# Performance work log

Hardware: AMD Instinct MI355X
Metric: run time of the kernel (lower is better)

## Reference

```python
import jax, jax.numpy as jnp
import numpy as np
import math

V = 32000      # vocab_size
D = 1024       # hidden_dims
T_MAX = 1024   # max_txt_len
L = 4          # n_layers
H = 8          # heads (fixed in CausalMHA)
HD = D // H
B, T = 2, 1024
EPS = 1e-5


def setup_inputs() -> dict:
    key = jax.random.key(0)
    ks = jax.random.split(key, 20)
    s = 0.02
    inp = {
        "x": jax.random.randint(ks[0], (B, T), 0, V, dtype=jnp.int64) if jax.config.read("jax_enable_x64") else jax.random.randint(ks[0], (B, T), 0, V, dtype=jnp.int32),
        "tok_emb": jax.random.normal(ks[1], (V, D), jnp.float32) * s,
        "pos_emb": jax.random.normal(ks[2], (1, T_MAX, D), jnp.float32) * s,
        "ln1_g": jnp.ones((L, D), jnp.float32),
        "ln1_b": jnp.zeros((L, D), jnp.float32),
        "wqkv": jax.random.normal(ks[3], (L, D, 3 * D), jnp.float32) * s,
        "bqkv": jnp.zeros((L, 3 * D), jnp.float32),
        "wo": jax.random.normal(ks[4], (L, D, D), jnp.float32) * s,
        "bo": jnp.zeros((L, D), jnp.float32),
        "ln2_g": jnp.ones((L, D), jnp.float32),
        "ln2_b": jnp.zeros((L, D), jnp.float32),
        "wfc": jax.random.normal(ks[5], (L, D, 4 * D), jnp.float32) * s,   # no bias
        "wfc2": jax.random.normal(ks[6], (L, 4 * D, D), jnp.float32) * s,  # no bias
        "fn_g": jnp.ones((D,), jnp.float32),
        "fn_b": jnp.zeros((D,), jnp.float32),
        "wout": jax.random.normal(ks[7], (D, V), jnp.float32) * s,
        "bout": jnp.zeros((V,), jnp.float32),
    }
    return inp


def _ln(x, g, b):
    mu = jnp.mean(x, axis=-1, keepdims=True)
    var = jnp.var(x, axis=-1, keepdims=True)
    return (x - mu) * jax.lax.rsqrt(var + EPS) * g + b


def _attn(xn, wqkv_l, bqkv_l, wo_l, bo_l):
    Bb, Tt, _ = xn.shape
    qkv = xn @ wqkv_l + bqkv_l                      # [B,T,3D]
    q, k, v = jnp.split(qkv, 3, axis=-1)
    q = q.reshape(Bb, Tt, H, HD)
    k = k.reshape(Bb, Tt, H, HD)
    v = v.reshape(Bb, Tt, H, HD)
    scores = jnp.einsum("bqhd,bkhd->bhqk", q, k) / math.sqrt(HD)
    mask = jnp.triu(jnp.ones((Tt, Tt), bool), k=1)   # True above diagonal
    scores = jnp.where(mask, jnp.float32(-jnp.inf), scores)
    att = jax.nn.softmax(scores, axis=-1)
    out = jnp.einsum("bhqk,bkhd->bqhd", att, v).reshape(Bb, Tt, D)
    return out @ wo_l + bo_l


def reference(x, tok_emb, pos_emb, ln1_g, ln1_b, wqkv, bqkv, wo, bo,
              ln2_g, ln2_b, wfc, wfc2, fn_g, fn_b, wout, bout):
    Tt = x.shape[1]
    h = tok_emb[x] + pos_emb[:, :Tt, :]              # [B,T,D]
    for i in range(L):
        h = h + _attn(_ln(h, ln1_g[i], ln1_b[i]), wqkv[i], bqkv[i], wo[i], bo[i])
        hn = _ln(h, ln2_g[i], ln2_b[i])
        h = h + jax.nn.gelu(hn @ wfc[i], approximate=False) @ wfc2[i]
    h = _ln(h, fn_g, fn_b)
    return h @ wout + bout                           # [B,T,V] logits
```

## Files before the change

kernel.cpp:

```cpp
#include <hip/hip_runtime.h>
#include <math.h>
#include <stdint.h>

#define D_  1024
#define T_  1024
#define H_  8
#define HD_ 128
#define L_  4
#define V_  32000
#define M_  2048

typedef __attribute__((ext_vector_type(4))) float f32x4;
typedef __attribute__((ext_vector_type(4))) short s16x4;
typedef __attribute__((ext_vector_type(8))) short s16x8;
typedef unsigned short u16;

__device__ __forceinline__ u16 f2bf(float f) {
  union { float f; uint32_t u; } c; c.f = f;
  uint32_t r = c.u + 0x7fffu + ((c.u >> 16) & 1u);
  return (u16)(r >> 16);
}
__device__ __forceinline__ float bf2f(u16 h) {
  union { uint32_t u; float f; } c; c.u = ((uint32_t)h) << 16;
  return c.f;
}
__device__ __forceinline__ float gelu_f(float x) {
  return 0.5f * x * (1.0f + erff(x * 0.70710678118654752f));
}

__device__ __forceinline__ void gload16(const u16* g, u16* l) {
  __builtin_amdgcn_global_load_lds(
      (const __attribute__((address_space(1))) void*)(uintptr_t)g,
      (__attribute__((address_space(3))) void*)(uint32_t)(uintptr_t)l,
      16, 0, 0);
}

template<int INF32>
__global__ __launch_bounds__(256)
void convT_kernel(const void* __restrict__ inv, u16* __restrict__ out,
                  int ldin, int ldout, long inZ, long outZ)
{
  __shared__ __align__(16) u16 tile[64][72];
  const int c0 = blockIdx.x << 6, r0 = blockIdx.y << 6;
  const int t = threadIdx.x;
  const int rr = t >> 2, cs = (t & 3) << 4;
  u16 tmp[16];
  if (INF32) {
    const float* in = (const float*)inv + (size_t)blockIdx.z * inZ;
    const float* p = in + (size_t)(r0 + rr) * ldin + c0 + cs;
#pragma unroll
    for (int q = 0; q < 4; ++q) {
      f32x4 v = *(const f32x4*)(p + q * 4);
#pragma unroll
      for (int j = 0; j < 4; ++j) tmp[q * 4 + j] = f2bf(v[j]);
    }
  } else {
    const u16* in = (const u16*)inv + (size_t)blockIdx.z * inZ;
    const u16* p = in + (size_t)(r0 + rr) * ldin + c0 + cs;
    s16x8 v0 = *(const s16x8*)(p);
    s16x8 v1 = *(const s16x8*)(p + 8);
#pragma unroll
    for (int j = 0; j < 8; ++j) { tmp[j] = (u16)v0[j]; tmp[8 + j] = (u16)v1[j]; }
  }
  *(s16x8*)&tile[rr][cs]     = *(const s16x8*)tmp;
  *(s16x8*)&tile[rr][cs + 8] = *(const s16x8*)(tmp + 8);
  __syncthreads();
  const int cr = t >> 2, rs = (t & 3) << 4;
  u16 o[16];
#pragma unroll
  for (int j = 0; j < 16; ++j) o[j] = tile[rs + j][cr];
  u16* op = out + (size_t)blockIdx.z * outZ + (size_t)(c0 + cr) * ldout + r0 + rs;
  *(s16x8*)op       = *(const s16x8*)o;
  *(s16x8*)(op + 8) = *(const s16x8*)(o + 8);
}

template<int TM, int ACT, int BIAS, int OUT, int MODE>
__global__ __launch_bounds__(256)
void gemm2(const u16* __restrict__ A, const u16* __restrict__ Bw,
           const float* __restrict__ bias, const float* __restrict__ res,
           void* __restrict__ Cv,
           int K, int lda, int ldb, int ldc, float scale,
           long sAb, long sAh, long sBb, long sBh, long sCb, long sCh)
{
  static_assert(TM == 64 || TM == 128, "tile");
  constexpr int WN  = (TM == 128) ? 2 : 4;
  constexpr int WNW = 128 / WN;
  constexpr int NJ  = WNW / 16;
  constexpr int AR  = TM / 64;

  const int bx = blockIdx.x, by = blockIdx.y, z = blockIdx.z;
  if (MODE == 1 && by > bx) return;
  const int m0 = bx * TM, n0 = by * 128;
  int ktiles = K >> 5;
  if (MODE == 2) { const int lim = (m0 + TM) >> 5; if (lim < ktiles) ktiles = lim; }

  const u16* Ab = A  + (size_t)(z >> 3) * sAb + (size_t)(z & 7) * sAh;
  const u16* Bb = Bw + (size_t)(z >> 3) * sBb + (size_t)(z & 7) * sBh;

  __shared__ __align__(16) u16 As[2][TM * 32];
  __shared__ __align__(16) u16 Bs[2][128 * 32];

  const int tid = threadIdx.x, lane = tid & 63, wave = tid >> 6;
  const int wm = wave / WN, wn = wave % WN;
  const int l15 = lane & 15, l4 = lane >> 4;
  const int srow = lane >> 2, scol = (lane & 3) << 3;

  f32x4 acc[4][NJ];
  const f32x4 z4 = {0.f, 0.f, 0.f, 0.f};
#pragma unroll
  for (int i = 0; i < 4; ++i)
#pragma unroll
    for (int j = 0; j < NJ; ++j) acc[i][j] = z4;

  auto stage = [&](int kt, int buf) {
    const int kc = (kt << 5) + scol;
#pragma unroll
    for (int r = 0; r < AR; ++r) {
      const int row = r * 64 + wave * 16;
      gload16(Ab + (size_t)(m0 + row + srow) * lda + kc, &As[buf][row * 32]);
    }
#pragma unroll
    for (int r = 0; r < 2; ++r) {
      const int row = r * 64 + wave * 16;
      gload16(Bb + (size_t)(n0 + row + srow) * ldb + kc, &Bs[buf][row * 32]);
    }
  };

  stage(0, 0);
  __syncthreads();

  for (int kt = 0; kt < ktiles; ++kt) {
    const int buf = kt & 1;
    if (kt + 1 < ktiles) stage(kt + 1, buf ^ 1);
    const u16* ap = &As[buf][(wm * 64 + l15) * 32 + (l4 << 3)];
    const u16* bp = &Bs[buf][(wn * WNW + l15) * 32 + (l4 << 3)];
    s16x8 af[4], bf[NJ];
#pragma unroll
    for (int i = 0; i < 4; ++i) af[i] = *(const s16x8*)(ap + i * (16 * 32));
#pragma unroll
    for (int j = 0; j < NJ; ++j) bf[j] = *(const s16x8*)(bp + j * (16 * 32));
#pragma unroll
    for (int i = 0; i < 4; ++i)
#pragma unroll
      for (int j = 0; j < NJ; ++j)
        acc[i][j] = __builtin_amdgcn_mfma_f32_16x16x32_bf16(af[i], bf[j], acc[i][j], 0, 0, 0);
    __syncthreads();
  }

  const size_t cbase = (size_t)(z >> 3) * sCb + (size_t)(z & 7) * sCh;
  float* Cf = (float*)Cv;
  u16*   Ch = (u16*)Cv;
#pragma unroll
  for (int i = 0; i < 4; ++i) {
    const int row0 = m0 + wm * 64 + i * 16 + l4 * 4;
#pragma unroll
    for (int j = 0; j < NJ; ++j) {
      const int col = n0 + wn * WNW + j * 16 + l15;
      const float bv = BIAS ? bias[col] : 0.0f;
#pragma unroll
      for (int r = 0; r < 4; ++r) {
        float v = acc[i][j][r] * scale + bv;
        if (ACT) v = gelu_f(v);
        const size_t idx = cbase + (size_t)(row0 + r) * ldc + col;
        if (OUT == 0)      Ch[idx] = f2bf(v);
        else if (OUT == 1) Cf[idx] = v;
        else               Cf[idx] = v + res[idx];
      }
    }
  }
}

__global__ __launch_bounds__(256)
void ln_bf16(const float* __restrict__ x, const float* __restrict__ g,
             const float* __restrict__ b, u16* __restrict__ y)
{
  __shared__ float red[8];
  const int row = blockIdx.x, tid = threadIdx.x;
  f32x4 v = *(const f32x4*)&x[(size_t)row * D_ + tid * 4];
  float s  = v[0] + v[1] + v[2] + v[3];
  float s2 = v[0]*v[0] + v[1]*v[1] + v[2]*v[2] + v[3]*v[3];
#pragma unroll
  for (int off = 32; off > 0; off >>= 1) {
    s  += __shfl_xor(s, off);
    s2 += __shfl_xor(s2, off);
  }
  if ((tid & 63) == 0) { red[tid >> 6] = s; red[4 + (tid >> 6)] = s2; }
  __syncthreads();
  s  = red[0] + red[1] + red[2] + red[3];
  s2 = red[4] + red[5] + red[6] + red[7];
  const float mean = s * (1.0f / D_);
  const float var  = s2 * (1.0f / D_) - mean * mean;
  const float rs   = rsqrtf(var + 1e-5f);
  f32x4 gg = *(const f32x4*)&g[tid * 4];
  f32x4 bb = *(const f32x4*)&b[tid * 4];
  u16 o[4];
#pragma unroll
  for (int j = 0; j < 4; ++j) o[j] = f2bf((v[j] - mean) * rs * gg[j] + bb[j]);
  *(s16x4*)&y[(size_t)row * D_ + tid * 4] = *(const s16x4*)o;
}

__global__ __launch_bounds__(256)
void softmax_bf16(u16* __restrict__ S)
{
  __shared__ float red[8];
  const int rI = blockIdx.x, tid = threadIdx.x;
  const int q = rI & (T_ - 1);
  u16* row = S + (size_t)rI * T_;
  s16x4 v = *(const s16x4*)&row[tid * 4];
  float s[4];
  float mx = -1e30f;
#pragma unroll
  for (int j = 0; j < 4; ++j) {
    const int c = tid * 4 + j;
    s[j] = (c <= q) ? bf2f((u16)v[j]) : -1e30f;
    mx = fmaxf(mx, s[j]);
  }
#pragma unroll
  for (int off = 32; off > 0; off >>= 1) mx = fmaxf(mx, __shfl_xor(mx, off));
  if ((tid & 63) == 0) red[tid >> 6] = mx;
  __syncthreads();
  mx = fmaxf(fmaxf(red[0], red[1]), fmaxf(red[2], red[3]));
  float p[4], sum = 0.f;
#pragma unroll
  for (int j = 0; j < 4; ++j) {
    p[j] = (tid * 4 + j <= q) ? __expf(s[j] - mx) : 0.f;
    sum += p[j];
  }
#pragma unroll
  for (int off = 32; off > 0; off >>= 1) sum += __shfl_xor(sum, off);
  if ((tid & 63) == 0) red[4 + (tid >> 6)] = sum;
  __syncthreads();
  sum = red[4] + red[5] + red[6] + red[7];
  const float inv = 1.0f / sum;
  u16 o[4];
#pragma unroll
  for (int j = 0; j < 4; ++j) o[j] = f2bf(p[j] * inv);
  *(s16x4*)&row[tid * 4] = *(const s16x4*)o;
}

__global__ __launch_bounds__(256)
void embed_kernel(const int* __restrict__ x, const float* __restrict__ tok,
                  const float* __restrict__ pos, float* __restrict__ h)
{
  const int row = blockIdx.x, tid = threadIdx.x;
  const int t = row & (T_ - 1);
  const int id = x[row];
  f32x4 a = *(const f32x4*)&tok[(size_t)id * D_ + tid * 4];
  f32x4 p = *(const f32x4*)&pos[(size_t)t * D_ + tid * 4];
  f32x4 o = {a[0] + p[0], a[1] + p[1], a[2] + p[2], a[3] + p[3]};
  *(f32x4*)&h[(size_t)row * D_ + tid * 4] = o;
}

extern "C" void kernel_launch(void* const* d_in, const int* in_sizes, int n_in,
                              void* d_out, int out_size, void* d_ws, size_t ws_size,
                              hipStream_t stream)
{
  (void)in_sizes; (void)n_in; (void)out_size; (void)ws_size;
  const int*   x     = (const int*)  d_in[0];
  const float* tok   = (const float*)d_in[1];
  const float* pos   = (const float*)d_in[2];
  const float* ln1_g = (const float*)d_in[3];
  const float* ln1_b = (const float*)d_in[4];
  const float* wqkv  = (const float*)d_in[5];
  const float* bqkv  = (const float*)d_in[6];
  const float* wo    = (const float*)d_in[7];
  const float* bo    = (const float*)d_in[8];
  const float* ln2_g = (const float*)d_in[9];
  const float* ln2_b = (const float*)d_in[10];
  const float* wfc   = (const float*)d_in[11];
  const float* wfc2  = (const float*)d_in[12];
  const float* fn_g  = (const float*)d_in[13];
  const float* fn_b  = (const float*)d_in[14];
  const float* wout  = (const float*)d_in[15];
  const float* bout  = (const float*)d_in[16];
  float* out = (float*)d_out;

  float* h  = (float*)d_ws;
  u16* xn   = (u16*)(h + (size_t)M_ * D_);
  u16* Wq   = xn  + (size_t)M_ * D_;
  u16* Wo   = Wq  + (size_t)3 * D_ * D_;
  u16* Wf1  = Wo  + (size_t)D_ * D_;
  u16* Wf2  = Wf1 + (size_t)4 * D_ * D_;
  u16* qkv  = Wf2 + (size_t)4 * D_ * D_;
  u16* Vt   = qkv + (size_t)M_ * 3 * D_;
  u16* S    = Vt  + (size_t)2 * T_ * D_;
  u16* WoutT = Wq;

  const long sQb = (long)T_ * 3 * D_;
  const long sSb = (long)8 * T_ * T_;
  const long sSh = (long)T_ * T_;
  const float iscale = 0.08838834764831845f;

  embed_kernel<<<M_, 256, 0, stream>>>(x, tok, pos, h);

  for (int l = 0; l < L_; ++l) {
    convT_kernel<1><<<dim3(48, 16, 1), 256, 0, stream>>>(
        wqkv + (size_t)l * D_ * 3 * D_, Wq, 3 * D_, D_, 0, 0);
    convT_kernel<1><<<dim3(16, 16, 1), 256, 0, stream>>>(
        wo + (size_t)l * D_ * D_, Wo, D_, D_, 0, 0);
    convT_kernel<1><<<dim3(64, 16, 1), 256, 0, stream>>>(
        wfc + (size_t)l * D_ * 4 * D_, Wf1, 4 * D_, D_, 0, 0);
    convT_kernel<1><<<dim3(16, 64, 1), 256, 0, stream>>>(
        wfc2 + (size_t)l * 4 * D_ * D_, Wf2, D_, 4 * D_, 0, 0);

    ln_bf16<<<M_, 256, 0, stream>>>(h, ln1_g + l * D_, ln1_b + l * D_, xn);
    gemm2<128, 0, 1, 0, 0><<<dim3(16, 24, 1), 256, 0, stream>>>(
        xn, Wq, bqkv + l * 3 * D_, nullptr, qkv,
        D_, D_, D_, 3 * D_, 1.0f, 0, 0, 0, 0, 0, 0);
    gemm2<128, 0, 0, 0, 1><<<dim3(8, 8, 16), 256, 0, stream>>>(
        qkv, qkv + D_, nullptr, nullptr, S,
        HD_, 3 * D_, 3 * D_, T_, iscale,
        sQb, (long)HD_, sQb, (long)HD_, sSb, sSh);
    softmax_bf16<<<16 * T_, 256, 0, stream>>>(S);
    convT_kernel<0><<<dim3(16, 16, 2), 256, 0, stream>>>(
        qkv + 2 * D_, Vt, 3 * D_, T_, (long)T_ * 3 * D_, (long)T_ * D_);
    gemm2<64, 0, 0, 0, 2><<<dim3(16, 1, 16), 256, 0, stream>>>(
        S, Vt, nullptr, nullptr, xn,
        T_, T_, T_, D_, 1.0f,
        sSb, sSh, (long)T_ * D_, (long)HD_ * T_, (long)T_ * D_, (long)HD_);
    gemm2<64, 0, 1, 2, 0><<<dim3(32, 8, 1), 256, 0, stream>>>(
        xn, Wo, bo + l * D_, h, h,
        D_, D_, D_, D_, 1.0f, 0, 0, 0, 0, 0, 0);
    ln_bf16<<<M_, 256, 0, stream>>>(h, ln2_g + l * D_, ln2_b + l * D_, xn);
    gemm2<128, 1, 0, 0, 0><<<dim3(16, 32, 1), 256, 0, stream>>>(
        xn, Wf1, nullptr, nullptr, S,
        D_, D_, D_, 4 * D_, 1.0f, 0, 0, 0, 0, 0, 0);
    gemm2<64, 0, 0, 2, 0><<<dim3(32, 8, 1), 256, 0, stream>>>(
        S, Wf2, nullptr, h, h,
        4 * D_, 4 * D_, 4 * D_, D_, 1.0f, 0, 0, 0, 0, 0, 0);
  }

  ln_bf16<<<M_, 256, 0, stream>>>(h, fn_g, fn_b, xn);
  convT_kernel<1><<<dim3(500, 16, 1), 256, 0, stream>>>(
      wout, WoutT, V_, D_, 0, 0);
  gemm2<128, 0, 1, 1, 0><<<dim3(16, 250, 1), 256, 0, stream>>>(
      xn, WoutT, bout, nullptr, out,
      D_, D_, D_, V_, 1.0f, 0, 0, 0, 0, 0, 0);
}
```

Baseline: 1.047 ms.

## Add 256x256 pipelined logits GEMM, swizzle workgroup order, wave-per-row softmax

Replaces the final vocab-projection GEMM with a dedicated 512-thread kernel that uses 256x256 tiles, a swizzled double-buffered LDS layout, interleaved global prefetch, and MFMA phases raised in priority. The goal is higher data reuse and better overlap on the largest GEMM. It also adds a workgroup-index swizzle to the generic GEMM for better L2 locality. Softmax now handles one row per wave with 16 elements per lane, which removes LDS reductions and block barriers. These changes add complexity and hardcoded shape assumptions, and the swizzle may unbalance the causal early-exit grids.

```diff
diff --git a/kernel.cpp b/kernel.cpp
--- a/kernel.cpp
+++ b/kernel.cpp
@@ -88,7 +88,14 @@
   constexpr int NJ  = WNW / 16;
   constexpr int AR  = TM / 64;
 
-  const int bx = blockIdx.x, by = blockIdx.y, z = blockIdx.z;
+  const int gx = gridDim.x, gy = gridDim.y;
+  int flat = (blockIdx.z * gy + blockIdx.y) * gx + blockIdx.x;
+  const int nwg = gx * gy * gridDim.z;
+  int swz = (flat & 7) * (nwg >> 3) + (flat >> 3);
+  const int bx = swz % gx; swz /= gx;
+  const int by = swz % gy;
+  const int z  = swz / gy;
+
   if (MODE == 1 && by > bx) return;
   const int m0 = bx * TM, n0 = by * 128;
   int ktiles = K >> 5;
@@ -166,6 +173,132 @@
         else if (OUT == 1) Cf[idx] = v;
         else               Cf[idx] = v + res[idx];
       }
+    }
+  }
+}
+
+__global__ __launch_bounds__(512, 2)
+void gemm8_logits(const u16* __restrict__ A, const u16* __restrict__ Bw,
+                  const float* __restrict__ bias, float* __restrict__ C)
+{
+  int flat = blockIdx.x;
+  int swz = (flat & 7) * 125 + (flat >> 3);
+  const int bx = swz & 7;
+  const int by = swz >> 3;
+  const int m0 = bx << 8, n0 = by << 8;
+
+  __shared__ __align__(16) u16 lds[65536];
+
+  const int tid = threadIdx.x, lane = tid & 63, wave = tid >> 6;
+  const int wm = wave >> 2, wn = wave & 3;
+  const int l15 = lane & 15, l4 = lane >> 4;
+
+  f32x4 acc[8][4];
+  const f32x4 z4 = {0.f, 0.f, 0.f, 0.f};
+#pragma unroll
+  for (int i = 0; i < 8; ++i)
+#pragma unroll
+    for (int j = 0; j < 4; ++j) acc[i][j] = z4;
+
+  auto stg = [&](const u16* G, int rowbase, int slot, int kt, int kh) {
+    if (kt >= 16) return;
+#pragma unroll
+    for (int r = 0; r < 2; ++r) {
+      const int u = r * 512 + (wave << 6) + lane;
+      const int rw = u >> 2, ks = u & 3;
+      const int ksw = ks ^ ((rw >> 1) & 3);
+      const u16* src = G + (size_t)(rowbase + rw) * 1024 + (kt << 6) + (kh << 5) + (ksw << 3);
+      gload16(src, &lds[slot + r * 4096 + (wave << 9)]);
+    }
+  };
+
+  s16x8 af[4], bfr[4];
+
+#define LDA4(bb, kk, mh)                                                      \
+  {                                                                           \
+    _Pragma("unroll") for (int f = 0; f < 4; ++f) {                           \
+      const int rw = wm * 128 + (mh) * 64 + f * 16 + l15;                     \
+      af[f] = *(const s16x8*)&lds[(bb) + (kk) * 8192 + rw * 32 +              \
+                                  ((l4 ^ ((rw >> 1) & 3)) << 3)];             \
+    }                                                                         \
+  }
+#define LDB4(bb, kk)                                                          \
+  {                                                                           \
+    _Pragma("unroll") for (int f = 0; f < 4; ++f) {                           \
+      const int rn = wn * 64 + f * 16 + l15;                                  \
+      bfr[f] = *(const s16x8*)&lds[(bb) + 16384 + (kk) * 8192 + rn * 32 +     \
+                                   ((l4 ^ ((rn >> 1) & 3)) << 3)];            \
+    }                                                                         \
+  }
+#define MFMA16(mh)                                                            \
+  {                                                                           \
+    __builtin_amdgcn_s_barrier();                                             \
+    asm volatile("s_waitcnt lgkmcnt(0)" ::: "memory");                        \
+    __builtin_amdgcn_sched_barrier(0);                                        \
+    __builtin_amdgcn_s_setprio(1);                                            \
+    _Pragma("unroll") for (int f = 0; f < 4; ++f)                             \
+      _Pragma("unroll") for (int nf = 0; nf < 4; ++nf)                        \
+        acc[(mh) * 4 + f][nf] = __builtin_amdgcn_mfma_f32_16x16x32_bf16(      \
+            af[f], bfr[nf], acc[(mh) * 4 + f][nf], 0, 0, 0);                  \
+    __builtin_amdgcn_s_setprio(0);                                            \
+  }
+#define BAR() __builtin_amdgcn_s_barrier()
+#define VM4() asm volatile("s_waitcnt vmcnt(4)" ::: "memory")
+
+  stg(A,  m0, 0,             0, 0);
+  stg(Bw, n0, 16384,         0, 0);
+  stg(A,  m0, 8192,          0, 1);
+  stg(Bw, n0, 16384 + 8192,  0, 1);
+  stg(A,  m0, 32768,         1, 0);
+  stg(Bw, n0, 32768 + 16384, 1, 0);
+  VM4();
+  BAR();
+
+  for (int i = 0; i < 8; ++i) {
+    const int t = 2 * i;
+    LDA4(0, 0, 0); LDB4(0, 0);
+    stg(A, m0, 32768 + 8192, t + 1, 1);
+    MFMA16(0); BAR();
+    LDA4(0, 0, 1);
+    stg(Bw, n0, 32768 + 24576, t + 1, 1);
+    MFMA16(1); BAR();
+    LDA4(0, 1, 0); LDB4(0, 1);
+    stg(A, m0, 0, t + 2, 0);
+    MFMA16(0); BAR();
+    LDA4(0, 1, 1);
+    stg(Bw, n0, 16384, t + 2, 0);
+    MFMA16(1); VM4(); BAR();
+    LDA4(32768, 0, 0); LDB4(32768, 0);
+    stg(A, m0, 8192, t + 2, 1);
+    MFMA16(0); BAR();
+    LDA4(32768, 0, 1);
+    stg(Bw, n0, 16384 + 8192, t + 2, 1);
+    MFMA16(1); BAR();
+    LDA4(32768, 1, 0); LDB4(32768, 1);
+    stg(A, m0, 32768, t + 3, 0);
+    MFMA16(0); BAR();
+    LDA4(32768, 1, 1);
+    stg(Bw, n0, 32768 + 16384, t + 3, 0);
+    MFMA16(1); VM4(); BAR();
+  }
+#undef LDA4
+#undef LDB4
+#undef MFMA16
+#undef BAR
+#undef VM4
+
+  float bv[4];
+#pragma unroll
+  for (int nf = 0; nf < 4; ++nf) bv[nf] = bias[n0 + wn * 64 + nf * 16 + l15];
+#pragma unroll
+  for (int mf = 0; mf < 8; ++mf) {
+    const int row0 = m0 + wm * 128 + mf * 16 + l4 * 4;
+#pragma unroll
+    for (int nf = 0; nf < 4; ++nf) {
+      const int col = n0 + wn * 64 + nf * 16 + l15;
+#pragma unroll
+      for (int r = 0; r < 4; ++r)
+        C[(size_t)(row0 + r) * V_ + col] = acc[mf][nf][r] + bv[nf];
     }
   }
 }
@@ -202,40 +335,40 @@
 __global__ __launch_bounds__(256)
 void softmax_bf16(u16* __restrict__ S)
 {
-  __shared__ float red[8];
-  const int rI = blockIdx.x, tid = threadIdx.x;
+  const int rI = blockIdx.x * 4 + (threadIdx.x >> 6);
+  const int lane = threadIdx.x & 63;
   const int q = rI & (T_ - 1);
   u16* row = S + (size_t)rI * T_;
-  s16x4 v = *(const s16x4*)&row[tid * 4];
-  float s[4];
+  s16x8 v0 = *(const s16x8*)&row[lane * 16];
+  s16x8 v1 = *(const s16x8*)&row[lane * 16 + 8];
+  float s[16];
   float mx = -1e30f;
 #pragma unroll
-  for (int j = 0; j < 4; ++j) {
-    const int c = tid * 4 + j;
-    s[j] = (c <= q) ? bf2f((u16)v[j]) : -1e30f;
+  for (int j = 0; j < 16; ++j) {
+    const int c = lane * 16 + j;
+    const u16 raw = (u16)(j < 8 ? v0[j] : v1[j - 8]);
+    s[j] = (c <= q) ? bf2f(raw) : -1e30f;
     mx = fmaxf(mx, s[j]);
   }
 #pragma unroll
   for (int off = 32; off > 0; off >>= 1) mx = fmaxf(mx, __shfl_xor(mx, off));
-  if ((tid & 63) == 0) red[tid >> 6] = mx;
-  __syncthreads();
-  mx = fmaxf(fmaxf(red[0], red[1]), fmaxf(red[2], red[3]));
-  float p[4], sum = 0.f;
-#pragma unroll
-  for (int j = 0; j < 4; ++j) {
-    p[j] = (tid * 4 + j <= q) ? __expf(s[j] - mx) : 0.f;
-    sum += p[j];
+  float sum = 0.f;
+#pragma unroll
+  for (int j = 0; j < 16; ++j) {
+    s[j] = (lane * 16 + j <= q) ? __expf(s[j] - mx) : 0.f;
+    sum += s[j];
   }
 #pragma unroll
   for (int off = 32; off > 0; off >>= 1) sum += __shfl_xor(sum, off);
-  if ((tid & 63) == 0) red[4 + (tid >> 6)] = sum;
-  __syncthreads();
-  sum = red[4] + red[5] + red[6] + red[7];
   const float inv = 1.0f / sum;
-  u16 o[4];
-#pragma unroll
-  for (int j = 0; j < 4; ++j) o[j] = f2bf(p[j] * inv);
-  *(s16x4*)&row[tid * 4] = *(const s16x4*)o;
+  s16x8 o0, o1;
+#pragma unroll
+  for (int j = 0; j < 8; ++j) {
+    o0[j] = (short)f2bf(s[j] * inv);
+    o1[j] = (short)f2bf(s[j + 8] * inv);
+  }
+  *(s16x8*)&row[lane * 16]     = o0;
+  *(s16x8*)&row[lane * 16 + 8] = o1;
 }
 
 __global__ __launch_bounds__(256)
@@ -311,7 +444,7 @@
         qkv, qkv + D_, nullptr, nullptr, S,
         HD_, 3 * D_, 3 * D_, T_, iscale,
         sQb, (long)HD_, sQb, (long)HD_, sSb, sSh);
-    softmax_bf16<<<16 * T_, 256, 0, stream>>>(S);
+    softmax_bf16<<<16 * T_ / 4, 256, 0, stream>>>(S);
     convT_kernel<0><<<dim3(16, 16, 2), 256, 0, stream>>>(
         qkv + 2 * D_, Vt, 3 * D_, T_, (long)T_ * 3 * D_, (long)T_ * D_);
     gemm2<64, 0, 0, 0, 2><<<dim3(16, 1, 16), 256, 0, stream>>>(
@@ -333,7 +466,5 @@
   ln_bf16<<<M_, 256, 0, stream>>>(h, fn_g, fn_b, xn);
   convT_kernel<1><<<dim3(500, 16, 1), 256, 0, stream>>>(
       wout, WoutT, V_, D_, 0, 0);
-  gemm2<128, 0, 1, 1, 0><<<dim3(16, 250, 1), 256, 0, stream>>>(
-      xn, WoutT, bout, nullptr, out,
-      D_, D_, D_, V_, 1.0f, 0, 0, 0, 0, 0, 0);
-}
+  gemm8_logits<<<1000, 512, 0, stream>>>(xn, WoutT, bout, out);
+}
```

New measurement: 996.7 us. 1.05x faster.
